# Kernel optimization log

Hardware: AMD Instinct MI355X
Metric: run time of the kernel (lower is better)

Reference implementation:

```python
import jax, jax.numpy as jnp
import numpy as np

TAU = 0.75

def normalize_W(W):
    n = jnp.linalg.norm(W)
    n = jax.nn.relu(n - 1.0) + 1.0
    return W / n

def setup_inputs() -> dict:
    key = jax.random.key(0)
    ks = jax.random.split(key, 14)
    C_in, C_out, K = 64, 128, 3
    B, L = 32, 4096
    nh = 64
    chunk_in_d = C_out * K            # 384
    D = C_in * (K + 2 * (C_out // C_in))  # 448
    r = lambda k, shp, s=1.0: jax.random.normal(k, shp, dtype=jnp.float32) * s
    W = normalize_W(r(ks[4], (D, 32)))
    return {
        "x": r(ks[0], (B, C_in, L)),
        "conv_weight": r(ks[1], (C_out, C_in, K), 0.1),
        "bias_param": r(ks[2], (C_out,), 0.1),
        "grads": r(ks[3], (C_out * C_in * K,), 0.1),
        "W": W,
        "ctrl_w": r(ks[5], (nh, chunk_in_d), 0.05),
        "ctrl_b": r(ks[6], (nh,), 0.05),
        "cw_w": r(ks[7], (K, nh), 0.05),
        "cw_b": r(ks[8], (K,), 0.05),
        "cb_w": r(ks[9], (C_out // C_in, nh), 0.05),
        "cb_b": r(ks[10], (C_out // C_in,), 0.05),
        "cf_w": r(ks[11], (C_out // C_in, nh), 0.05),
        "cf_b": r(ks[12], (C_out // C_in,), 0.05),
        "trigger": 1,
    }

def fw_chunks(grads, W, ctrl_w, ctrl_b, cw_w, cw_b, cb_w, cb_b, cf_w, cf_b, trigger, n_chunks):
    g = grads.reshape(n_chunks, -1)                    # (C_in, C_out*K)
    rep = jax.nn.silu(g @ ctrl_w.T + ctrl_b)           # (C_in, nh)
    w = rep @ cw_w.T + cw_b                            # (C_in, K)
    b = rep @ cb_w.T + cb_b                            # (C_in, C_out/C_in)
    f = rep @ cf_w.T + cf_b                            # (C_in, C_out/C_in)
    q = jnp.concatenate([w.ravel(), b.ravel(), f.ravel()])  # (D,)  first call: no q_ema
    W_upd = W
    if trigger == 1:  # codebook attention / top-k / scatter-EMA path
        dim = w.shape[0]
        att = jax.nn.softmax(q @ W / 0.5)              # (32,)
        v, idx = jax.lax.top_k(att, 2)
        ww = W[:, idx]                                 # (D, 2)
        old_w = ww @ idx.astype(jnp.float32)[:, None]  # (D, 1) -- indices used as weights, as in source
        s_att = jnp.zeros((att.shape[0],), jnp.float32).at[idx].set(v)
        W_contrib = old_w @ s_att[None, :]             # (D, 32)
        mask = jnp.ones(W.shape, jnp.float32).at[:, idx].set(TAU)
        W_upd = normalize_W(mask * W + (1.0 - mask) * W_contrib)
        nw, nb, nf = w.shape[1], b.shape[1], f.shape[1]
        o_w = old_w[: nw * dim]
        o_b = old_w[nw * dim : (nw + nb) * dim]
        o_f = old_w[-nf * dim :]
        w = TAU * w + (1.0 - TAU) * o_w.reshape(w.shape)
        b = TAU * b + (1.0 - TAU) * o_b.reshape(b.shape)
        f = TAU * f + (1.0 - TAU) * o_f.reshape(f.shape)
    f = f.reshape(-1)[None, :, None]                   # (1, C_out, 1)
    return w[None], b.reshape(-1), f, W_upd

def reference(x, conv_weight, bias_param, grads, W, ctrl_w, ctrl_b, cw_w, cw_b, cb_w, cb_b, cf_w, cf_b, trigger):
    n_chunks = conv_weight.shape[1]  # in_channels
    w, b, f, W_upd = fw_chunks(grads, W, ctrl_w, ctrl_b, cw_w, cw_b, cb_w, cb_b, cf_w, cf_b, trigger, n_chunks)
    cw = conv_weight * w                               # (C_out, C_in, K)
    pad = ((conv_weight.shape[2] - 1) * 1 + 1) // 2    # receptive_field // 2
    conv_out = jax.lax.conv_general_dilated(
        x, cw, window_strides=(1,), padding=[(pad, pad)], rhs_dilation=(1,),
        dimension_numbers=("NCH", "OIH", "NCH"))
    conv_out = conv_out + (bias_param * b)[None, :, None]
    out = f * conv_out                                 # (B, C_out, L)
    return out, W_upd
```

## Files before the change

kernel.cpp:

```cpp
#include <hip/hip_runtime.h>
#include <hip/hip_bf16.h>
#include <math.h>

#define TAU 0.75f

typedef _Float16 half8 __attribute__((ext_vector_type(8)));
typedef float    f32x4 __attribute__((ext_vector_type(4)));

#define LDS_BARRIER() do {                                   \
    asm volatile("s_waitcnt lgkmcnt(0)" ::: "memory");       \
    __builtin_amdgcn_s_barrier();                            \
    asm volatile("" ::: "memory");                           \
} while (0)

#define WS_Q     0
#define WS_NORM2 448
#define WS_SCALE 449
#define WS_V01   450
#define WS_I01   452
#define WS_WQ    456
#define WS_FSC   648
#define WS_BADD  776
#define WS_OW    904
#define WS_WF16  1352

__global__ __launch_bounds__(256) void k1_rep_q(
    const float* __restrict__ grads, const float* __restrict__ ctrl_w,
    const float* __restrict__ ctrl_b,
    const float* __restrict__ cw_w, const float* __restrict__ cw_b,
    const float* __restrict__ cb_w, const float* __restrict__ cb_b,
    const float* __restrict__ cf_w, const float* __restrict__ cf_b,
    const float* __restrict__ W, float* __restrict__ ws)
{
    const int t = threadIdx.x;
    if (blockIdx.x == 64) {
        __shared__ float red[256];
        float ss = 0.f;
        for (int e = t; e < 3584; e += 256) {
            const float4 w4 = ((const float4*)W)[e];
            ss += w4.x * w4.x + w4.y * w4.y + w4.z * w4.z + w4.w * w4.w;
        }
        red[t] = ss; __syncthreads();
        for (int s = 128; s > 0; s >>= 1) { if (t < s) red[t] += red[t + s]; __syncthreads(); }
        if (t == 0) ws[WS_NORM2] = red[0];
        return;
    }
    const int c = blockIdx.x;
    __shared__ float gS[384];
    __shared__ float repS[64];
    if (t < 96) ((float4*)gS)[t] = ((const float4*)(grads + c * 384))[t];
    __syncthreads();
    {
        const int h = t >> 2, sub = t & 3;
        const float4* wa = (const float4*)(ctrl_w + h * 384) + sub * 24;
        const float4* ga = (const float4*)gS + sub * 24;
        float dot = 0.f;
        #pragma unroll
        for (int d = 0; d < 24; d++) {
            const float4 a = ga[d], b = wa[d];
            dot += a.x * b.x + a.y * b.y + a.z * b.z + a.w * b.w;
        }
        dot += __shfl_xor(dot, 1);
        dot += __shfl_xor(dot, 2);
        if (sub == 0) {
            const float z = dot + ctrl_b[h];
            repS[h] = z / (1.f + expf(-z));
        }
    }
    __syncthreads();
    if (t < 7) {
        const float* wv; float bias; int e;
        if (t < 3)      { wv = cw_w + t * 64;       bias = cw_b[t];     e = 3 * c + t; }
        else if (t < 5) { const int j = t - 3; wv = cb_w + j * 64; bias = cb_b[j]; e = 192 + 2 * c + j; }
        else            { const int j = t - 5; wv = cf_w + j * 64; bias = cf_b[j]; e = 320 + 2 * c + j; }
        float dot = 0.f;
        #pragma unroll 8
        for (int h = 0; h < 64; h++) dot += repS[h] * wv[h];
        ws[WS_Q + e] = dot + bias;
    }
}

__global__ __launch_bounds__(256) void k2_small(
    const float* __restrict__ W, const float* __restrict__ bias_param,
    const int* __restrict__ trigger, float* __restrict__ ws)
{
    __shared__ float qS[448], owS[448], sS[32], sW[4][32], red[256];
    __shared__ int   idxS[2];
    __shared__ float vS[2];
    const int t = threadIdx.x;
    const int wv = t >> 6, lane = t & 63;
    const int trig = trigger[0];

    for (int e = t; e < 448; e += 256) qS[e] = ws[WS_Q + e];
    __syncthreads();

    {
        const int m = lane & 31, half = lane >> 5;
        float s = 0.f;
        const int base = wv * 112;
        #pragma unroll 4
        for (int it = 0; it < 56; it++) {
            const int d = base + it * 2 + half;
            s += qS[d] * W[d * 32 + m];
        }
        s += __shfl_xor(s, 32);
        if (lane < 32) sW[wv][lane] = s;
    }
    __syncthreads();
    if (t < 32) sS[t] = 2.f * (sW[0][t] + sW[1][t] + sW[2][t] + sW[3][t]);
    __syncthreads();
    if (t == 0) {
        float mx = sS[0];
        for (int m = 1; m < 32; m++) mx = fmaxf(mx, sS[m]);
        float sum = 0.f; float att[32];
        for (int m = 0; m < 32; m++) { att[m] = expf(sS[m] - mx); sum += att[m]; }
        const float inv = 1.f / sum;
        int i0 = 0; float v0 = att[0];
        for (int m = 1; m < 32; m++) if (att[m] > v0) { v0 = att[m]; i0 = m; }
        int i1 = -1; float v1 = -1.f;
        for (int m = 0; m < 32; m++) { if (m == i0) continue; if (att[m] > v1) { v1 = att[m]; i1 = m; } }
        idxS[0] = i0; idxS[1] = i1; vS[0] = v0 * inv; vS[1] = v1 * inv;
    }
    __syncthreads();
    const int i0 = idxS[0], i1 = idxS[1];
    const float v0 = vS[0], v1 = vS[1];

    float corr = 0.f;
    for (int d = t; d < 448; d += 256) {
        const float w0 = W[d * 32 + i0], w1 = W[d * 32 + i1];
        const float ow = (trig == 1) ? (w0 * (float)i0 + w1 * (float)i1) : 0.f;
        owS[d] = ow;
        if (trig == 1) {
            const float n0 = TAU * w0 + 0.25f * ow * v0;
            const float n1 = TAU * w1 + 0.25f * ow * v1;
            corr += n0 * n0 - w0 * w0 + n1 * n1 - w1 * w1;
        }
    }
    red[t] = corr; __syncthreads();
    for (int s = 128; s > 0; s >>= 1) { if (t < s) red[t] += red[t + s]; __syncthreads(); }
    if (t == 0) {
        const float n = sqrtf(fmaxf(ws[WS_NORM2] + red[0], 0.f));
        ws[WS_SCALE] = 1.f / fmaxf(n, 1.f);
        ws[WS_V01] = v0; ws[WS_V01 + 1] = v1;
        ((int*)ws)[WS_I01] = i0; ((int*)ws)[WS_I01 + 1] = i1;
    }

    if (t < 192) ws[WS_WQ + t] = (trig == 1) ? (TAU * qS[t] + 0.25f * owS[t]) : qS[t];
    for (int o = t; o < 128; o += 256) {
        float bb = qS[192 + o], ff = qS[320 + o];
        if (trig == 1) {
            bb = TAU * bb + 0.25f * owS[192 + o];
            ff = TAU * ff + 0.25f * owS[320 + o];
        }
        ws[WS_FSC + o]  = ff;
        ws[WS_BADD + o] = ff * bias_param[o] * bb;
    }
    for (int d = t; d < 448; d += 256) ws[WS_OW + d] = owS[d];
}

__global__ __launch_bounds__(256) void k3_finalize(
    const float* __restrict__ W, const float* __restrict__ conv_weight,
    const int* __restrict__ trigger, const float* __restrict__ ws,
    float* __restrict__ W_out, _Float16* __restrict__ wf_out)
{
    const int g = blockIdx.x * 256 + threadIdx.x;
    const int trig = trigger[0];
    if (g < 14336) {
        const float wv = W[g];
        float wn = wv;
        if (trig == 1) {
            const int d = g >> 5, m = g & 31;
            const int i0 = ((const int*)ws)[WS_I01], i1 = ((const int*)ws)[WS_I01 + 1];
            if (m == i0)      wn = TAU * wv + 0.25f * ws[WS_OW + d] * ws[WS_V01];
            else if (m == i1) wn = TAU * wv + 0.25f * ws[WS_OW + d] * ws[WS_V01 + 1];
            wn *= ws[WS_SCALE];
        }
        W_out[g] = wn;
    } else {
        const int e2 = g - 14336;
        const int o   = e2 / 192;
        const int rem = e2 - o * 192;
        const int i   = rem / 3;
        const int kk  = rem - i * 3;
        wf_out[(kk * 128 + o) * 64 + i] = (_Float16)(conv_weight[e2] * ws[WS_WQ + rem]);
    }
}

__global__ __launch_bounds__(256, 2) void conv_mfma(
    const float* __restrict__ x, const _Float16* __restrict__ wf,
    const float* __restrict__ fsc, const float* __restrict__ badd,
    float* __restrict__ out)
{
    __shared__ __align__(16) _Float16 xs[2][66 * 72];

    const int t     = threadIdx.x;
    const int wv    = t >> 6;
    const int lane  = t & 63;
    const int lrow  = lane & 15;
    const int lgrp  = lane >> 4;
    const int b     = blockIdx.x >> 4;
    const int lbase = (blockIdx.x & 15) * 256;
    const int obase = wv * 32;

    const float* xb = x + (size_t)b * 64 * 4096;
    const int ci = t & 3;
    const int ir = t >> 2;
    const int ei = t & 63;
    const int side = (t >> 6) & 1;

    half8 Wf[2][2][3];
    #pragma unroll
    for (int of = 0; of < 2; of++)
        #pragma unroll
        for (int ch = 0; ch < 2; ch++)
            #pragma unroll
            for (int kk = 0; kk < 3; kk++)
                Wf[of][ch][kk] = *(const half8*)(wf + ((kk * 128 + obase + of * 16 + lrow) * 64 + ch * 32 + lgrp * 8));

    float fs_[2], ba_[2];
    #pragma unroll
    for (int of = 0; of < 2; of++) {
        const int o = obase + of * 16 + lrow;
        fs_[of] = fsc[o]; ba_[of] = badd[o];
    }

    float4 xrA[4], xrB[4];
    float  xeA = 0.f, xeB = 0.f;

#define STAGE_LOAD(xr, xe, lb) do {                                          \
    _Pragma("unroll")                                                        \
    for (int j = 0; j < 4; j++)                                              \
        (xr)[j] = *(const float4*)(xb + (size_t)ir * 4096 + (lb) + ci * 16 + j * 4); \
    (xe) = 0.f;                                                              \
    if (t < 128) {                                                           \
        const int l_ = side ? ((lb) + 64) : ((lb) - 1);                      \
        if (l_ >= 0 && l_ < 4096) (xe) = xb[(size_t)ei * 4096 + l_];         \
    }                                                                        \
} while (0)

#define STAGE_WRITE(buf, xr, xe) do {                                        \
    _Pragma("unroll")                                                        \
    for (int j = 0; j < 4; j++) {                                            \
        _Float16* p_ = (buf) + (ci * 16 + j * 4 + 1) * 72 + ir;              \
        p_[0]   = (_Float16)(xr)[j].x;                                       \
        p_[72]  = (_Float16)(xr)[j].y;                                       \
        p_[144] = (_Float16)(xr)[j].z;                                       \
        p_[216] = (_Float16)(xr)[j].w;                                       \
    }                                                                        \
    if (t < 128) (buf)[(side ? 65 : 0) * 72 + ei] = (_Float16)(xe);          \
} while (0)

#define COMPUTE_STORE(buf, lb) do {                                          \
    f32x4 acc[2][4];                                                         \
    _Pragma("unroll")                                                        \
    for (int of = 0; of < 2; of++)                                           \
        _Pragma("unroll")                                                    \
        for (int lf = 0; lf < 4; lf++) acc[of][lf] = (f32x4)0.f;             \
    _Pragma("unroll")                                                        \
    for (int ch = 0; ch < 2; ch++) {                                         \
        _Pragma("unroll")                                                    \
        for (int kk = 0; kk < 3; kk++) {                                     \
            half8 Xf[4];                                                     \
            _Pragma("unroll")                                                \
            for (int lf = 0; lf < 4; lf++)                                   \
                Xf[lf] = *(const half8*)((buf) + (lf * 16 + lrow + kk) * 72 + ch * 32 + lgrp * 8); \
            _Pragma("unroll")                                                \
            for (int of = 0; of < 2; of++)                                   \
                _Pragma("unroll")                                            \
                for (int lf = 0; lf < 4; lf++)                               \
                    acc[of][lf] = __builtin_amdgcn_mfma_f32_16x16x32_f16(Xf[lf], Wf[of][ch][kk], acc[of][lf], 0, 0, 0); \
        }                                                                    \
    }                                                                        \
    _Pragma("unroll")                                                        \
    for (int of = 0; of < 2; of++) {                                         \
        const int o_ = obase + of * 16 + lrow;                               \
        float* orow_ = out + ((size_t)(b * 128 + o_)) * 4096 + (lb) + lgrp * 4; \
        _Pragma("unroll")                                                    \
        for (int lf = 0; lf < 4; lf++) {                                     \
            float4 r_;                                                       \
            r_.x = fs_[of] * acc[of][lf][0] + ba_[of];                       \
            r_.y = fs_[of] * acc[of][lf][1] + ba_[of];                       \
            r_.z = fs_[of] * acc[of][lf][2] + ba_[of];                       \
            r_.w = fs_[of] * acc[of][lf][3] + ba_[of];                       \
            *(float4*)(orow_ + lf * 16) = r_;                                \
        }                                                                    \
    }                                                                        \
} while (0)

    STAGE_LOAD(xrA, xeA, lbase);
    STAGE_WRITE(xs[0], xrA, xeA);
    STAGE_LOAD(xrB, xeB, lbase + 64);
    LDS_BARRIER();

    STAGE_LOAD(xrA, xeA, lbase + 128);
    COMPUTE_STORE(xs[0], lbase);
    STAGE_WRITE(xs[1], xrB, xeB);
    LDS_BARRIER();

    STAGE_LOAD(xrB, xeB, lbase + 192);
    COMPUTE_STORE(xs[1], lbase + 64);
    STAGE_WRITE(xs[0], xrA, xeA);
    LDS_BARRIER();

    COMPUTE_STORE(xs[0], lbase + 128);
    STAGE_WRITE(xs[1], xrB, xeB);
    LDS_BARRIER();

    COMPUTE_STORE(xs[1], lbase + 192);

#undef STAGE_LOAD
#undef STAGE_WRITE
#undef COMPUTE_STORE
}

extern "C" void kernel_launch(void* const* d_in, const int* in_sizes, int n_in,
                              void* d_out, int out_size, void* d_ws, size_t ws_size,
                              hipStream_t stream) {
    const float* x           = (const float*)d_in[0];
    const float* conv_weight = (const float*)d_in[1];
    const float* bias_param  = (const float*)d_in[2];
    const float* grads       = (const float*)d_in[3];
    const float* W           = (const float*)d_in[4];
    const float* ctrl_w      = (const float*)d_in[5];
    const float* ctrl_b      = (const float*)d_in[6];
    const float* cw_w        = (const float*)d_in[7];
    const float* cw_b        = (const float*)d_in[8];
    const float* cb_w        = (const float*)d_in[9];
    const float* cb_b        = (const float*)d_in[10];
    const float* cf_w        = (const float*)d_in[11];
    const float* cf_b        = (const float*)d_in[12];
    const int*   trigger     = (const int*)d_in[13];

    float* out   = (float*)d_out;
    float* W_out = out + (size_t)32 * 128 * 4096;
    float* ws    = (float*)d_ws;
    _Float16* wfp = (_Float16*)(ws + WS_WF16);
    float* fsc   = ws + WS_FSC;
    float* badd  = ws + WS_BADD;

    k1_rep_q<<<65, 256, 0, stream>>>(grads, ctrl_w, ctrl_b, cw_w, cw_b,
                                     cb_w, cb_b, cf_w, cf_b, W, ws);
    k2_small<<<1, 256, 0, stream>>>(W, bias_param, trigger, ws);
    k3_finalize<<<152, 256, 0, stream>>>(W, conv_weight, trigger, ws, W_out, wfp);
    conv_mfma<<<512, 256, 0, stream>>>(x, wfp, fsc, badd, out);
}
```

Baseline: 41.85 us.

## Fuse prelude kernels into cooperative kernel, swizzle LDS, fold output scale into weights

The three small prelude kernels are merged into one cooperative kernel that uses grid.sync() between phases, which removes two launch gaps. The per-channel output scale f is folded into the fp16 conv weights, so the epilogue only adds the bias. The LDS tile gets an XOR swizzle to reduce bank conflicts on the MFMA operand reads. The second stage load is issued earlier to overlap the two loads. Cooperative launch has its own overhead and grid barriers, and folding f into fp16 weights changes rounding slightly.

```diff
diff --git a/kernel.cpp b/kernel.cpp
--- a/kernel.cpp
+++ b/kernel.cpp
@@ -1,6 +1,9 @@
 #include <hip/hip_runtime.h>
 #include <hip/hip_bf16.h>
+#include <hip/hip_cooperative_groups.h>
 #include <math.h>
+
+namespace cg = cooperative_groups;
 
 #define TAU 0.75f
 
@@ -12,6 +15,8 @@
     __builtin_amdgcn_s_barrier();                            \
     asm volatile("" ::: "memory");                           \
 } while (0)
+
+#define SWZ(row) ((((row) >> 3) & 7) << 3)
 
 #define WS_Q     0
 #define WS_NORM2 448
@@ -24,17 +29,28 @@
 #define WS_OW    904
 #define WS_WF16  1352
 
-__global__ __launch_bounds__(256) void k1_rep_q(
+__global__ __launch_bounds__(256) void prelude_coop(
     const float* __restrict__ grads, const float* __restrict__ ctrl_w,
     const float* __restrict__ ctrl_b,
     const float* __restrict__ cw_w, const float* __restrict__ cw_b,
     const float* __restrict__ cb_w, const float* __restrict__ cb_b,
     const float* __restrict__ cf_w, const float* __restrict__ cf_b,
-    const float* __restrict__ W, float* __restrict__ ws)
+    const float* __restrict__ W, const float* __restrict__ bias_param,
+    const float* __restrict__ conv_weight, const int* __restrict__ trigger,
+    float* __restrict__ ws, float* __restrict__ W_out,
+    _Float16* __restrict__ wf_out)
 {
-    const int t = threadIdx.x;
-    if (blockIdx.x == 64) {
-        __shared__ float red[256];
+    cg::grid_group grid = cg::this_grid();
+    const int t = threadIdx.x, bid = blockIdx.x;
+    const int trig = trigger[0];
+
+    __shared__ float gS[384];
+    __shared__ float repS[64];
+    __shared__ float qS[448], owS[448], sS[32], sW[4][32], red[256];
+    __shared__ int   idxS[2];
+    __shared__ float vS[2];
+
+    if (bid == 64) {
         float ss = 0.f;
         for (int e = t; e < 3584; e += 256) {
             const float4 w4 = ((const float4*)W)[e];
@@ -43,153 +59,138 @@
         red[t] = ss; __syncthreads();
         for (int s = 128; s > 0; s >>= 1) { if (t < s) red[t] += red[t + s]; __syncthreads(); }
         if (t == 0) ws[WS_NORM2] = red[0];
-        return;
+    } else {
+        const int c = bid;
+        if (t < 96) ((float4*)gS)[t] = ((const float4*)(grads + c * 384))[t];
+        __syncthreads();
+        {
+            const int h = t >> 2, sub = t & 3;
+            const float4* wa = (const float4*)(ctrl_w + h * 384) + sub * 24;
+            const float4* ga = (const float4*)gS + sub * 24;
+            float dot = 0.f;
+            #pragma unroll
+            for (int d = 0; d < 24; d++) {
+                const float4 a = ga[d], b = wa[d];
+                dot += a.x * b.x + a.y * b.y + a.z * b.z + a.w * b.w;
+            }
+            dot += __shfl_xor(dot, 1);
+            dot += __shfl_xor(dot, 2);
+            if (sub == 0) {
+                const float z = dot + ctrl_b[h];
+                repS[h] = z / (1.f + expf(-z));
+            }
+        }
+        __syncthreads();
+        if (t < 7) {
+            const float* wv; float bias; int e;
+            if (t < 3)      { wv = cw_w + t * 64;       bias = cw_b[t];     e = 3 * c + t; }
+            else if (t < 5) { const int j = t - 3; wv = cb_w + j * 64; bias = cb_b[j]; e = 192 + 2 * c + j; }
+            else            { const int j = t - 5; wv = cf_w + j * 64; bias = cf_b[j]; e = 320 + 2 * c + j; }
+            float dot = 0.f;
+            #pragma unroll 8
+            for (int h = 0; h < 64; h++) dot += repS[h] * wv[h];
+            ws[WS_Q + e] = dot + bias;
+        }
     }
-    const int c = blockIdx.x;
-    __shared__ float gS[384];
-    __shared__ float repS[64];
-    if (t < 96) ((float4*)gS)[t] = ((const float4*)(grads + c * 384))[t];
-    __syncthreads();
-    {
-        const int h = t >> 2, sub = t & 3;
-        const float4* wa = (const float4*)(ctrl_w + h * 384) + sub * 24;
-        const float4* ga = (const float4*)gS + sub * 24;
-        float dot = 0.f;
-        #pragma unroll
-        for (int d = 0; d < 24; d++) {
-            const float4 a = ga[d], b = wa[d];
-            dot += a.x * b.x + a.y * b.y + a.z * b.z + a.w * b.w;
-        }
-        dot += __shfl_xor(dot, 1);
-        dot += __shfl_xor(dot, 2);
-        if (sub == 0) {
-            const float z = dot + ctrl_b[h];
-            repS[h] = z / (1.f + expf(-z));
-        }
+
+    grid.sync();
+
+    if (bid == 64) {
+        const int wv = t >> 6, lane = t & 63;
+        for (int e = t; e < 448; e += 256) qS[e] = ws[WS_Q + e];
+        __syncthreads();
+        {
+            const int m = lane & 31, half = lane >> 5;
+            float s = 0.f;
+            const int base = wv * 112;
+            #pragma unroll 4
+            for (int it = 0; it < 56; it++) {
+                const int d = base + it * 2 + half;
+                s += qS[d] * W[d * 32 + m];
+            }
+            s += __shfl_xor(s, 32);
+            if (lane < 32) sW[wv][lane] = s;
+        }
+        __syncthreads();
+        if (t < 32) sS[t] = 2.f * (sW[0][t] + sW[1][t] + sW[2][t] + sW[3][t]);
+        __syncthreads();
+        if (t == 0) {
+            float mx = sS[0];
+            for (int m = 1; m < 32; m++) mx = fmaxf(mx, sS[m]);
+            float sum = 0.f; float att[32];
+            for (int m = 0; m < 32; m++) { att[m] = expf(sS[m] - mx); sum += att[m]; }
+            const float inv = 1.f / sum;
+            int i0 = 0; float v0 = att[0];
+            for (int m = 1; m < 32; m++) if (att[m] > v0) { v0 = att[m]; i0 = m; }
+            int i1 = -1; float v1 = -1.f;
+            for (int m = 0; m < 32; m++) { if (m == i0) continue; if (att[m] > v1) { v1 = att[m]; i1 = m; } }
+            idxS[0] = i0; idxS[1] = i1; vS[0] = v0 * inv; vS[1] = v1 * inv;
+        }
+        __syncthreads();
+        const int i0 = idxS[0], i1 = idxS[1];
+        const float v0 = vS[0], v1 = vS[1];
+
+        float corr = 0.f;
+        for (int d = t; d < 448; d += 256) {
+            const float w0 = W[d * 32 + i0], w1 = W[d * 32 + i1];
+            const float ow = (trig == 1) ? (w0 * (float)i0 + w1 * (float)i1) : 0.f;
+            owS[d] = ow;
+            if (trig == 1) {
+                const float n0 = TAU * w0 + 0.25f * ow * v0;
+                const float n1 = TAU * w1 + 0.25f * ow * v1;
+                corr += n0 * n0 - w0 * w0 + n1 * n1 - w1 * w1;
+            }
+        }
+        red[t] = corr; __syncthreads();
+        for (int s = 128; s > 0; s >>= 1) { if (t < s) red[t] += red[t + s]; __syncthreads(); }
+        if (t == 0) {
+            const float n = sqrtf(fmaxf(ws[WS_NORM2] + red[0], 0.f));
+            ws[WS_SCALE] = 1.f / fmaxf(n, 1.f);
+            ws[WS_V01] = v0; ws[WS_V01 + 1] = v1;
+            ((int*)ws)[WS_I01] = i0; ((int*)ws)[WS_I01 + 1] = i1;
+        }
+        if (t < 192) ws[WS_WQ + t] = (trig == 1) ? (TAU * qS[t] + 0.25f * owS[t]) : qS[t];
+        for (int o = t; o < 128; o += 256) {
+            float bb = qS[192 + o], ff = qS[320 + o];
+            if (trig == 1) {
+                bb = TAU * bb + 0.25f * owS[192 + o];
+                ff = TAU * ff + 0.25f * owS[320 + o];
+            }
+            ws[WS_FSC + o]  = ff;
+            ws[WS_BADD + o] = ff * bias_param[o] * bb;
+        }
+        for (int d = t; d < 448; d += 256) ws[WS_OW + d] = owS[d];
     }
-    __syncthreads();
-    if (t < 7) {
-        const float* wv; float bias; int e;
-        if (t < 3)      { wv = cw_w + t * 64;       bias = cw_b[t];     e = 3 * c + t; }
-        else if (t < 5) { const int j = t - 3; wv = cb_w + j * 64; bias = cb_b[j]; e = 192 + 2 * c + j; }
-        else            { const int j = t - 5; wv = cf_w + j * 64; bias = cf_b[j]; e = 320 + 2 * c + j; }
-        float dot = 0.f;
-        #pragma unroll 8
-        for (int h = 0; h < 64; h++) dot += repS[h] * wv[h];
-        ws[WS_Q + e] = dot + bias;
+
+    grid.sync();
+
+    for (int g = bid * 256 + t; g < 38912; g += 65 * 256) {
+        if (g < 14336) {
+            const float wv = W[g];
+            float wn = wv;
+            if (trig == 1) {
+                const int d = g >> 5, m = g & 31;
+                const int i0 = ((const int*)ws)[WS_I01], i1 = ((const int*)ws)[WS_I01 + 1];
+                if (m == i0)      wn = TAU * wv + 0.25f * ws[WS_OW + d] * ws[WS_V01];
+                else if (m == i1) wn = TAU * wv + 0.25f * ws[WS_OW + d] * ws[WS_V01 + 1];
+                wn *= ws[WS_SCALE];
+            }
+            W_out[g] = wn;
+        } else {
+            const int e2 = g - 14336;
+            const int o   = e2 / 192;
+            const int rem = e2 - o * 192;
+            const int i   = rem / 3;
+            const int kk  = rem - i * 3;
+            wf_out[(kk * 128 + o) * 64 + i] =
+                (_Float16)(conv_weight[e2] * ws[WS_WQ + rem] * ws[WS_FSC + o]);
+        }
     }
 }
 
-__global__ __launch_bounds__(256) void k2_small(
-    const float* __restrict__ W, const float* __restrict__ bias_param,
-    const int* __restrict__ trigger, float* __restrict__ ws)
-{
-    __shared__ float qS[448], owS[448], sS[32], sW[4][32], red[256];
-    __shared__ int   idxS[2];
-    __shared__ float vS[2];
-    const int t = threadIdx.x;
-    const int wv = t >> 6, lane = t & 63;
-    const int trig = trigger[0];
-
-    for (int e = t; e < 448; e += 256) qS[e] = ws[WS_Q + e];
-    __syncthreads();
-
-    {
-        const int m = lane & 31, half = lane >> 5;
-        float s = 0.f;
-        const int base = wv * 112;
-        #pragma unroll 4
-        for (int it = 0; it < 56; it++) {
-            const int d = base + it * 2 + half;
-            s += qS[d] * W[d * 32 + m];
-        }
-        s += __shfl_xor(s, 32);
-        if (lane < 32) sW[wv][lane] = s;
-    }
-    __syncthreads();
-    if (t < 32) sS[t] = 2.f * (sW[0][t] + sW[1][t] + sW[2][t] + sW[3][t]);
-    __syncthreads();
-    if (t == 0) {
-        float mx = sS[0];
-        for (int m = 1; m < 32; m++) mx = fmaxf(mx, sS[m]);
-        float sum = 0.f; float att[32];
-        for (int m = 0; m < 32; m++) { att[m] = expf(sS[m] - mx); sum += att[m]; }
-        const float inv = 1.f / sum;
-        int i0 = 0; float v0 = att[0];
-        for (int m = 1; m < 32; m++) if (att[m] > v0) { v0 = att[m]; i0 = m; }
-        int i1 = -1; float v1 = -1.f;
-        for (int m = 0; m < 32; m++) { if (m == i0) continue; if (att[m] > v1) { v1 = att[m]; i1 = m; } }
-        idxS[0] = i0; idxS[1] = i1; vS[0] = v0 * inv; vS[1] = v1 * inv;
-    }
-    __syncthreads();
-    const int i0 = idxS[0], i1 = idxS[1];
-    const float v0 = vS[0], v1 = vS[1];
-
-    float corr = 0.f;
-    for (int d = t; d < 448; d += 256) {
-        const float w0 = W[d * 32 + i0], w1 = W[d * 32 + i1];
-        const float ow = (trig == 1) ? (w0 * (float)i0 + w1 * (float)i1) : 0.f;
-        owS[d] = ow;
-        if (trig == 1) {
-            const float n0 = TAU * w0 + 0.25f * ow * v0;
-            const float n1 = TAU * w1 + 0.25f * ow * v1;
-            corr += n0 * n0 - w0 * w0 + n1 * n1 - w1 * w1;
-        }
-    }
-    red[t] = corr; __syncthreads();
-    for (int s = 128; s > 0; s >>= 1) { if (t < s) red[t] += red[t + s]; __syncthreads(); }
-    if (t == 0) {
-        const float n = sqrtf(fmaxf(ws[WS_NORM2] + red[0], 0.f));
-        ws[WS_SCALE] = 1.f / fmaxf(n, 1.f);
-        ws[WS_V01] = v0; ws[WS_V01 + 1] = v1;
-        ((int*)ws)[WS_I01] = i0; ((int*)ws)[WS_I01 + 1] = i1;
-    }
-
-    if (t < 192) ws[WS_WQ + t] = (trig == 1) ? (TAU * qS[t] + 0.25f * owS[t]) : qS[t];
-    for (int o = t; o < 128; o += 256) {
-        float bb = qS[192 + o], ff = qS[320 + o];
-        if (trig == 1) {
-            bb = TAU * bb + 0.25f * owS[192 + o];
-            ff = TAU * ff + 0.25f * owS[320 + o];
-        }
-        ws[WS_FSC + o]  = ff;
-        ws[WS_BADD + o] = ff * bias_param[o] * bb;
-    }
-    for (int d = t; d < 448; d += 256) ws[WS_OW + d] = owS[d];
-}
-
-__global__ __launch_bounds__(256) void k3_finalize(
-    const float* __restrict__ W, const float* __restrict__ conv_weight,
-    const int* __restrict__ trigger, const float* __restrict__ ws,
-    float* __restrict__ W_out, _Float16* __restrict__ wf_out)
-{
-    const int g = blockIdx.x * 256 + threadIdx.x;
-    const int trig = trigger[0];
-    if (g < 14336) {
-        const float wv = W[g];
-        float wn = wv;
-        if (trig == 1) {
-            const int d = g >> 5, m = g & 31;
-            const int i0 = ((const int*)ws)[WS_I01], i1 = ((const int*)ws)[WS_I01 + 1];
-            if (m == i0)      wn = TAU * wv + 0.25f * ws[WS_OW + d] * ws[WS_V01];
-            else if (m == i1) wn = TAU * wv + 0.25f * ws[WS_OW + d] * ws[WS_V01 + 1];
-            wn *= ws[WS_SCALE];
-        }
-        W_out[g] = wn;
-    } else {
-        const int e2 = g - 14336;
-        const int o   = e2 / 192;
-        const int rem = e2 - o * 192;
-        const int i   = rem / 3;
-        const int kk  = rem - i * 3;
-        wf_out[(kk * 128 + o) * 64 + i] = (_Float16)(conv_weight[e2] * ws[WS_WQ + rem]);
-    }
-}
-
 __global__ __launch_bounds__(256, 2) void conv_mfma(
     const float* __restrict__ x, const _Float16* __restrict__ wf,
-    const float* __restrict__ fsc, const float* __restrict__ badd,
-    float* __restrict__ out)
+    const float* __restrict__ badd, float* __restrict__ out)
 {
     __shared__ __align__(16) _Float16 xs[2][66 * 72];
 
@@ -217,12 +218,10 @@
             for (int kk = 0; kk < 3; kk++)
                 Wf[of][ch][kk] = *(const half8*)(wf + ((kk * 128 + obase + of * 16 + lrow) * 64 + ch * 32 + lgrp * 8));
 
-    float fs_[2], ba_[2];
+    float ba_[2];
     #pragma unroll
-    for (int of = 0; of < 2; of++) {
-        const int o = obase + of * 16 + lrow;
-        fs_[of] = fsc[o]; ba_[of] = badd[o];
-    }
+    for (int of = 0; of < 2; of++)
+        ba_[of] = badd[obase + of * 16 + lrow];
 
     float4 xrA[4], xrB[4];
     float  xeA = 0.f, xeB = 0.f;
@@ -241,13 +240,16 @@
 #define STAGE_WRITE(buf, xr, xe) do {                                        \
     _Pragma("unroll")                                                        \
     for (int j = 0; j < 4; j++) {                                            \
-        _Float16* p_ = (buf) + (ci * 16 + j * 4 + 1) * 72 + ir;              \
-        p_[0]   = (_Float16)(xr)[j].x;                                       \
-        p_[72]  = (_Float16)(xr)[j].y;                                       \
-        p_[144] = (_Float16)(xr)[j].z;                                       \
-        p_[216] = (_Float16)(xr)[j].w;                                       \
-    }                                                                        \
-    if (t < 128) (buf)[(side ? 65 : 0) * 72 + ei] = (_Float16)(xe);          \
+        const int r0_ = ci * 16 + j * 4 + 1;                                 \
+        (buf)[(r0_ + 0) * 72 + (ir ^ SWZ(r0_ + 0))] = (_Float16)(xr)[j].x;   \
+        (buf)[(r0_ + 1) * 72 + (ir ^ SWZ(r0_ + 1))] = (_Float16)(xr)[j].y;   \
+        (buf)[(r0_ + 2) * 72 + (ir ^ SWZ(r0_ + 2))] = (_Float16)(xr)[j].z;   \
+        (buf)[(r0_ + 3) * 72 + (ir ^ SWZ(r0_ + 3))] = (_Float16)(xr)[j].w;   \
+    }                                                                        \
+    if (t < 128) {                                                           \
+        const int re_ = side ? 65 : 0;                                       \
+        (buf)[re_ * 72 + (ei ^ SWZ(re_))] = (_Float16)(xe);                  \
+    }                                                                        \
 } while (0)
 
 #define COMPUTE_STORE(buf, lb) do {                                          \
@@ -262,8 +264,10 @@
         for (int kk = 0; kk < 3; kk++) {                                     \
             half8 Xf[4];                                                     \
             _Pragma("unroll")                                                \
-            for (int lf = 0; lf < 4; lf++)                                   \
-                Xf[lf] = *(const half8*)((buf) + (lf * 16 + lrow + kk) * 72 + ch * 32 + lgrp * 8); \
+            for (int lf = 0; lf < 4; lf++) {                                 \
+                const int rr_ = lf * 16 + lrow + kk;                         \
+                Xf[lf] = *(const half8*)((buf) + rr_ * 72 + ((ch * 32 + lgrp * 8) ^ SWZ(rr_))); \
+            }                                                                \
             _Pragma("unroll")                                                \
             for (int of = 0; of < 2; of++)                                   \
                 _Pragma("unroll")                                            \
@@ -278,18 +282,18 @@
         _Pragma("unroll")                                                    \
         for (int lf = 0; lf < 4; lf++) {                                     \
             float4 r_;                                                       \
-            r_.x = fs_[of] * acc[of][lf][0] + ba_[of];                       \
-            r_.y = fs_[of] * acc[of][lf][1] + ba_[of];                       \
-            r_.z = fs_[of] * acc[of][lf][2] + ba_[of];                       \
-            r_.w = fs_[of] * acc[of][lf][3] + ba_[of];                       \
+            r_.x = acc[of][lf][0] + ba_[of];                                 \
+            r_.y = acc[of][lf][1] + ba_[of];                                 \
+            r_.z = acc[of][lf][2] + ba_[of];                                 \
+            r_.w = acc[of][lf][3] + ba_[of];                                 \
             *(float4*)(orow_ + lf * 16) = r_;                                \
         }                                                                    \
     }                                                                        \
 } while (0)
 
     STAGE_LOAD(xrA, xeA, lbase);
+    STAGE_LOAD(xrB, xeB, lbase + 64);
     STAGE_WRITE(xs[0], xrA, xeA);
-    STAGE_LOAD(xrB, xeB, lbase + 64);
     LDS_BARRIER();
 
     STAGE_LOAD(xrA, xeA, lbase + 128);
@@ -335,12 +339,17 @@
     float* W_out = out + (size_t)32 * 128 * 4096;
     float* ws    = (float*)d_ws;
     _Float16* wfp = (_Float16*)(ws + WS_WF16);
-    float* fsc   = ws + WS_FSC;
     float* badd  = ws + WS_BADD;
 
-    k1_rep_q<<<65, 256, 0, stream>>>(grads, ctrl_w, ctrl_b, cw_w, cw_b,
-                                     cb_w, cb_b, cf_w, cf_b, W, ws);
-    k2_small<<<1, 256, 0, stream>>>(W, bias_param, trigger, ws);
-    k3_finalize<<<152, 256, 0, stream>>>(W, conv_weight, trigger, ws, W_out, wfp);
-    conv_mfma<<<512, 256, 0, stream>>>(x, wfp, fsc, badd, out);
+    void* args[] = {
+        (void*)&grads, (void*)&ctrl_w, (void*)&ctrl_b,
+        (void*)&cw_w, (void*)&cw_b, (void*)&cb_w, (void*)&cb_b,
+        (void*)&cf_w, (void*)&cf_b, (void*)&W, (void*)&bias_param,
+        (void*)&conv_weight, (void*)&trigger, (void*)&ws, (void*)&W_out,
+        (void*)&wfp
+    };
+    hipLaunchCooperativeKernel((void*)prelude_coop, dim3(65), dim3(256),
+                               args, 0, stream);
+
+    conv_mfma<<<512, 256, 0, stream>>>(x, wfp, badd, out);
 }
```

New measurement: 73.19 us. +74.9%, slower.
